# Kernel tuning notes

Hardware: AMD Instinct MI355X
Metric: run time of the kernel (lower is better)

## Reference

```python
import jax, jax.numpy as jnp
import numpy as np

B = 64            # graphs
N0 = 1024         # nodes per graph at level 0
DEG = 16          # avg degree
D = 128
NS = [1024, 820, 656, 525, 420, 336]  # ceil(0.8*n) cascade


def gcn(x, src, dst, valid, W, b, num_nodes):
    # x: [N,D]; src/dst: [E] int; valid: [E] float mask; W: [D,D]; b: [D]
    x = x @ W.T + b
    deg = jax.ops.segment_sum(valid, src, num_segments=num_nodes) + 1.0  # +1 self loop
    dis = jax.lax.rsqrt(deg)
    norm = dis[src] * dis[dst] * valid
    agg = jax.ops.segment_sum(norm[:, None] * x[src], dst, num_segments=num_nodes)
    return agg + (dis * dis)[:, None] * x  # self-loop term


def topk_pool(x, src, dst, valid, w, n, k):
    # PyG TopKPooling: score = tanh((x.w)/||w||); keep top ceil(ratio*n) per graph
    s = jnp.tanh((x @ w) / jnp.linalg.norm(w))
    _, idx = jax.lax.top_k(s.reshape(B, n), k)                    # [B,k] local ids
    perm = (idx + (jnp.arange(B) * n)[:, None]).reshape(-1)       # global ids
    xn = x[perm] * s[perm][:, None]
    new_id = jnp.full((B * n,), -1, jnp.int32).at[perm].set(jnp.arange(B * k, dtype=jnp.int32))
    ns_, nd_ = new_id[src], new_id[dst]
    v = valid * ((ns_ >= 0) & (nd_ >= 0)).astype(jnp.float32)
    return xn, jnp.maximum(ns_, 0), jnp.maximum(nd_, 0), v


def setup_inputs() -> dict:
    key = jax.random.key(0)
    ks = jax.random.split(key, 32)
    x = jax.random.normal(ks[0], (B * N0, D), jnp.float32)
    eg = N0 * DEG  # edges per graph
    local = jax.random.randint(ks[1], (2, B, eg), 0, N0, jnp.int32)
    edge_index = (local + (jnp.arange(B, dtype=jnp.int32) * N0)[None, :, None]).reshape(2, -1)
    batch = jnp.repeat(jnp.arange(B, dtype=jnp.int32), N0)
    sc = 1.0 / np.sqrt(D)
    inp = {"x": x, "edge_index": edge_index, "batch": batch}
    for i in range(1, 6):
        inp[f"c{i}w"] = jax.random.normal(ks[2 * i], (D, D), jnp.float32) * sc
        inp[f"c{i}b"] = jnp.zeros((D,), jnp.float32)
        inp[f"p{i}w"] = jax.random.normal(ks[2 * i + 1], (D,), jnp.float32) * sc
    inp["l1w"] = jax.random.normal(ks[20], (128, 256), jnp.float32) / np.sqrt(256)
    inp["l1b"] = jnp.zeros((128,), jnp.float32)
    inp["l2w"] = jax.random.normal(ks[21], (64, 128), jnp.float32) * sc
    inp["l2b"] = jnp.zeros((64,), jnp.float32)
    inp["l3w"] = jax.random.normal(ks[22], (2, 64), jnp.float32) / np.sqrt(64)
    inp["l3b"] = jnp.zeros((2,), jnp.float32)
    return inp


def reference(x, edge_index, batch,
              c1w, c1b, p1w, c2w, c2b, p2w, c3w, c3b, p3w,
              c4w, c4b, p4w, c5w, c5b, p5w,
              l1w, l1b, l2w, l2b, l3w, l3b):
    src, dst = edge_index[0], edge_index[1]
    valid = jnp.ones(src.shape, jnp.float32)
    layers = [(c1w, c1b, p1w), (c2w, c2b, p2w), (c3w, c3b, p3w),
              (c4w, c4b, p4w), (c5w, c5b, p5w)]
    reads = []
    for i, (cw, cb, pw) in enumerate(layers):
        n, k = NS[i], NS[i + 1]
        x = jax.nn.relu(gcn(x, src, dst, valid, cw, cb, B * n))
        x, src, dst, valid = topk_pool(x, src, dst, valid, pw, n, k)
        xk = x.reshape(B, k, D)
        reads.append(jnp.concatenate([xk.max(axis=1), xk.mean(axis=1)], axis=1))
    h = reads[0] + reads[1] + reads[2] + reads[3] + reads[4]   # [B,256]
    h = jax.nn.relu(h @ l1w.T + l1b)
    # dropout is identity in eval mode
    h = jax.nn.relu(h @ l2w.T + l2b)
    return jax.nn.log_softmax(h @ l3w.T + l3b, axis=-1)       # [B,2]
```

## Files before the change

### kernel.cpp

```cpp
#include <hip/hip_runtime.h>
#include <math.h>

#define NB 64
#define DIM 128
#define ETOT 1048576
#define EPG 16384
#define EPT 16
#define WRS 192
#define XRS 96

static const int NS_H[6] = {1024, 820, 656, 525, 420, 336};

__global__ __launch_bounds__(1024) void init_kernel(const int* __restrict__ ei,
                                  int* __restrict__ src, int* __restrict__ dst,
                                  int2* __restrict__ epack, int* __restrict__ eoff,
                                  int* __restrict__ cnt, float* __restrict__ dinv,
                                  float* __restrict__ invn, const float* __restrict__ pw0,
                                  float* __restrict__ hsum) {
    __shared__ int hs[1024], hc[1024], cur[1024];
    __shared__ float dv[1024];
    __shared__ float shf[128];
    __shared__ int wsum[16];
    int g = blockIdx.x, t = threadIdx.x;
    int lane = t & 63, wv = t >> 6;
    hs[t] = 0; hc[t] = 0;
    if (t < 256) hsum[g * 256 + t] = 0.f;
    __syncthreads();
    int b0 = g * EPG;
    int sr[EPT], dr[EPT];
#pragma unroll
    for (int q = 0; q < EPT; q++) {
        int e = b0 + q * 1024 + t;
        int s = ei[e], d = ei[ETOT + e];
        sr[q] = s; dr[q] = d;
        src[e] = s; dst[e] = d;
        atomicAdd(&hs[s & 1023], 1);
        atomicAdd(&hc[d & 1023], 1);
    }
    __syncthreads();
    int v = hc[t];
    dv[t] = rsqrtf((float)hs[t] + 1.0f);
    int s = v;
#pragma unroll
    for (int off = 1; off < 64; off <<= 1) {
        int u = __shfl_up(s, off, 64);
        if (lane >= off) s += u;
    }
    if (lane == 63) wsum[wv] = s;
    __syncthreads();
    if (wv == 0) {
        int ws = (lane < 16) ? wsum[lane] : 0;
#pragma unroll
        for (int off = 1; off < 16; off <<= 1) {
            int u = __shfl_up(ws, off, 64);
            if (lane >= off) ws += u;
        }
        if (lane < 16) wsum[lane] = ws;
    }
    __syncthreads();
    int excl = b0 + s + ((wv > 0) ? wsum[wv - 1] : 0) - v;
    eoff[g * 1024 + t] = excl;
    cnt[g * 1024 + t] = v;
    dinv[g * 1024 + t] = dv[t];
    cur[t] = excl;
    __syncthreads();
#pragma unroll
    for (int q = 0; q < EPT; q++) {
        int sl = sr[q] & 1023, dl = dr[q] & 1023;
        int pos = atomicAdd(&cur[dl], 1);
        epack[pos] = make_int2(sr[q], __float_as_int(dv[sl] * dv[dl]));
    }
    if (g == 0) {
        if (t < 128) shf[t] = pw0[t] * pw0[t];
        __syncthreads();
        for (int q = 64; q > 0; q >>= 1) {
            if (t < q) shf[t] += shf[t + q];
            __syncthreads();
        }
        if (t == 0) invn[0] = rsqrtf(shf[0]);
    }
}

__global__ __launch_bounds__(256) void linear_kernel(const float* __restrict__ x,
                              const float* __restrict__ W, const float* __restrict__ b,
                              float* __restrict__ y, int N) {
    __shared__ float Wt[32 * WRS];
    __shared__ float xT[32 * XRS];
    int tid = threadIdx.x;
    int base = blockIdx.x * 64;
    int nf = tid & 15;
    int u  = tid >> 4;
    float acc[4][8];
    {
        float bv[8];
#pragma unroll
        for (int f = 0; f < 8; f++) bv[f] = b[u * 8 + f];
#pragma unroll
        for (int i = 0; i < 4; i++)
#pragma unroll
            for (int f = 0; f < 8; f++) acc[i][f] = bv[f];
    }
    for (int kb = 0; kb < 4; kb++) {
        __syncthreads();
#pragma unroll
        for (int q = 0; q < 4; q++) {
            int i = q * 256 + tid;
            int dq = i >> 7;
            int r = i & 127;
            int s = (r >> 3) * 12 + (r & 7);
            float4 wv = *(const float4*)(W + r * 128 + kb * 32 + dq * 4);
            Wt[(dq * 4 + 0) * WRS + s] = wv.x;
            Wt[(dq * 4 + 1) * WRS + s] = wv.y;
            Wt[(dq * 4 + 2) * WRS + s] = wv.z;
            Wt[(dq * 4 + 3) * WRS + s] = wv.w;
        }
#pragma unroll
        for (int q = 0; q < 2; q++) {
            int i = q * 256 + tid;
            int dq = i >> 6;
            int r = i & 63;
            int s = (r >> 3) * 12 + (r & 7);
            float4 xv = *(const float4*)(x + (size_t)(base + r) * DIM + kb * 32 + dq * 4);
            xT[(dq * 4 + 0) * XRS + s] = xv.x;
            xT[(dq * 4 + 1) * XRS + s] = xv.y;
            xT[(dq * 4 + 2) * XRS + s] = xv.z;
            xT[(dq * 4 + 3) * XRS + s] = xv.w;
        }
        __syncthreads();
#pragma unroll 4
        for (int d = 0; d < 32; d++) {
            float4 xv = *(const float4*)&xT[d * XRS + (nf >> 1) * 12 + (nf & 1) * 4];
            float4 wa = *(const float4*)&Wt[d * WRS + u * 12];
            float4 wb = *(const float4*)&Wt[d * WRS + u * 12 + 4];
            float xs[4] = {xv.x, xv.y, xv.z, xv.w};
            float ws[8] = {wa.x, wa.y, wa.z, wa.w, wb.x, wb.y, wb.z, wb.w};
#pragma unroll
            for (int i = 0; i < 4; i++)
#pragma unroll
                for (int f = 0; f < 8; f++)
                    acc[i][f] += xs[i] * ws[f];
        }
    }
#pragma unroll
    for (int i = 0; i < 4; i++) {
        int nd = base + nf * 4 + i;
        float* yp = y + (size_t)nd * DIM + u * 8;
        *(float4*)(yp + 0) = make_float4(acc[i][0], acc[i][1], acc[i][2], acc[i][3]);
        *(float4*)(yp + 4) = make_float4(acc[i][4], acc[i][5], acc[i][6], acc[i][7]);
    }
}

__global__ void fused_agg_kernel(const float* __restrict__ xL, const int2* __restrict__ epack,
                                 const int* __restrict__ eoff, const int* __restrict__ cnt,
                                 const float* __restrict__ dinv,
                                 const float* __restrict__ pw, const float* __restrict__ invn,
                                 float* __restrict__ xA, float* __restrict__ score, int n) {
    int t = threadIdx.x;
    int g = blockIdx.x % NB;
    int chunk = blockIdx.x / NB;
    int ln = chunk * 8 + (t >> 5);
    if (ln >= n) return;
    int node = g * n + ln;
    int lane = t & 31;
    float dsn = dinv[node];
    float4 sv = ((const float4*)(xL + (size_t)node * DIM))[lane];
    float w0 = dsn * dsn;
    float4 a0 = make_float4(sv.x * w0, sv.y * w0, sv.z * w0, sv.w * w0);
    float4 a1 = make_float4(0.f, 0.f, 0.f, 0.f);
    float4 a2 = make_float4(0.f, 0.f, 0.f, 0.f);
    float4 a3 = make_float4(0.f, 0.f, 0.f, 0.f);
    int s0 = eoff[node], s1 = s0 + cnt[node];
    int j = s0;
    int2 e0, e1, e2, e3;
    if (j + 3 < s1) { e0 = epack[j]; e1 = epack[j + 1]; e2 = epack[j + 2]; e3 = epack[j + 3]; }
    for (; j + 7 < s1; j += 4) {
        int2 f0 = epack[j + 4], f1 = epack[j + 5], f2 = epack[j + 6], f3 = epack[j + 7];
        float4 x0 = ((const float4*)(xL + (size_t)e0.x * DIM))[lane];
        float4 x1 = ((const float4*)(xL + (size_t)e1.x * DIM))[lane];
        float4 x2 = ((const float4*)(xL + (size_t)e2.x * DIM))[lane];
        float4 x3 = ((const float4*)(xL + (size_t)e3.x * DIM))[lane];
        float n0 = __int_as_float(e0.y), n1 = __int_as_float(e1.y);
        float n2 = __int_as_float(e2.y), n3 = __int_as_float(e3.y);
        a0.x += n0 * x0.x; a0.y += n0 * x0.y; a0.z += n0 * x0.z; a0.w += n0 * x0.w;
        a1.x += n1 * x1.x; a1.y += n1 * x1.y; a1.z += n1 * x1.z; a1.w += n1 * x1.w;
        a2.x += n2 * x2.x; a2.y += n2 * x2.y; a2.z += n2 * x2.z; a2.w += n2 * x2.w;
        a3.x += n3 * x3.x; a3.y += n3 * x3.y; a3.z += n3 * x3.z; a3.w += n3 * x3.w;
        e0 = f0; e1 = f1; e2 = f2; e3 = f3;
    }
    if (j + 3 < s1) {
        float4 x0 = ((const float4*)(xL + (size_t)e0.x * DIM))[lane];
        float4 x1 = ((const float4*)(xL + (size_t)e1.x * DIM))[lane];
        float4 x2 = ((const float4*)(xL + (size_t)e2.x * DIM))[lane];
        float4 x3 = ((const float4*)(xL + (size_t)e3.x * DIM))[lane];
        float n0 = __int_as_float(e0.y), n1 = __int_as_float(e1.y);
        float n2 = __int_as_float(e2.y), n3 = __int_as_float(e3.y);
        a0.x += n0 * x0.x; a0.y += n0 * x0.y; a0.z += n0 * x0.z; a0.w += n0 * x0.w;
        a1.x += n1 * x1.x; a1.y += n1 * x1.y; a1.z += n1 * x1.z; a1.w += n1 * x1.w;
        a2.x += n2 * x2.x; a2.y += n2 * x2.y; a2.z += n2 * x2.z; a2.w += n2 * x2.w;
        a3.x += n3 * x3.x; a3.y += n3 * x3.y; a3.z += n3 * x3.z; a3.w += n3 * x3.w;
        j += 4;
    }
    for (; j < s1; j++) {
        int2 eq = epack[j];
        float nq = __int_as_float(eq.y);
        float4 xq = ((const float4*)(xL + (size_t)eq.x * DIM))[lane];
        a0.x += nq * xq.x; a0.y += nq * xq.y; a0.z += nq * xq.z; a0.w += nq * xq.w;
    }
    float4 acc = make_float4(fmaxf(a0.x + a1.x + a2.x + a3.x, 0.f),
                             fmaxf(a0.y + a1.y + a2.y + a3.y, 0.f),
                             fmaxf(a0.z + a1.z + a2.z + a3.z, 0.f),
                             fmaxf(a0.w + a1.w + a2.w + a3.w, 0.f));
    ((float4*)(xA + (size_t)node * DIM))[lane] = acc;
    float4 pv = ((const float4*)pw)[lane];
    float dot = acc.x * pv.x + acc.y * pv.y + acc.z * pv.z + acc.w * pv.w;
    for (int off = 16; off >= 1; off >>= 1) dot += __shfl_xor(dot, off, 32);
    if (lane == 0) score[node] = tanhf(dot * invn[0]);
}

__global__ __launch_bounds__(1024) void pool_kernel(const float* __restrict__ score,
                              const float* __restrict__ xA, float* __restrict__ xn,
                              float* __restrict__ h, int* __restrict__ src,
                              int* __restrict__ dst, int2* __restrict__ epack,
                              int* __restrict__ eoff, int* __restrict__ cnt,
                              float* __restrict__ dinv, const float* __restrict__ pwN,
                              float* __restrict__ invn, int n, int k, int last,
                              const float* __restrict__ l1w, const float* __restrict__ l1b,
                              const float* __restrict__ l2w, const float* __restrict__ l2b,
                              const float* __restrict__ l3w, const float* __restrict__ l3b,
                              float* __restrict__ out) {
    __shared__ float keyS[2][1024];
    __shared__ int idxS[2][1024];
    __shared__ int nid[1024];
    __shared__ float4 smax[32][33];
    __shared__ float4 ssum[32][33];
    __shared__ int hs[1024], hc[1024], cur[1024];
    __shared__ float dv[1024];
    __shared__ float shf[128];
    __shared__ int wsum[16];
    __shared__ float hr[256], h1[128], h2[64], lz[2];
    int g = blockIdx.x, t = threadIdx.x;
    int lane = t & 63, wv = t >> 6;
    int b0 = g * EPG, gn = g * n, gk = g * k;
    float k_r = (t < n) ? score[g * n + t] : -2.0f;
    int i_r = t;
    hs[t] = 0; hc[t] = 0;
    int se[EPT], de[EPT];
    if (!last) {
#pragma unroll
        for (int q = 0; q < EPT; q++) {
            int e = b0 + q * 1024 + t;
            se[q] = src[e];
            de[q] = dst[e];
        }
    }
    int par = 0;
    for (unsigned ksz = 2; ksz <= 1024; ksz <<= 1) {
        for (unsigned jj = ksz >> 1; jj > 0; jj >>= 1) {
            float kq; int iq;
            if (jj >= 64) {
                keyS[par][t] = k_r; idxS[par][t] = i_r;
                __syncthreads();
                kq = keyS[par][t ^ jj]; iq = idxS[par][t ^ jj];
                par ^= 1;
            } else {
                kq = __shfl_xor(k_r, (int)jj, 64);
                iq = __shfl_xor(i_r, (int)jj, 64);
            }
            bool mineFirst = (k_r > kq) || (k_r == kq && i_r < iq);
            bool up = ((t & ksz) == 0);
            bool iAmLower = ((t & jj) == 0);
            bool keepMine = (iAmLower == up) ? mineFirst : !mineFirst;
            if (!keepMine) { k_r = kq; i_r = iq; }
        }
    }
    keyS[0][t] = k_r; idxS[0][t] = i_r;
    nid[i_r] = (t < (unsigned)k) ? t : -1;
    __syncthreads();
    int lane4 = t & 31;
    int ch = t >> 5;
    float4 mx = make_float4(-INFINITY, -INFINITY, -INFINITY, -INFINITY);
    float4 sm = make_float4(0.f, 0.f, 0.f, 0.f);
    for (int j = ch; j < k; j += 32) {
        int row = idxS[0][j];
        float sval = keyS[0][j];
        float4 vv = ((const float4*)(xA + ((size_t)g * n + row) * DIM))[lane4];
        vv.x *= sval; vv.y *= sval; vv.z *= sval; vv.w *= sval;
        if (!last) ((float4*)(xn + ((size_t)g * k + j) * DIM))[lane4] = vv;
        mx.x = fmaxf(mx.x, vv.x); mx.y = fmaxf(mx.y, vv.y);
        mx.z = fmaxf(mx.z, vv.z); mx.w = fmaxf(mx.w, vv.w);
        sm.x += vv.x; sm.y += vv.y; sm.z += vv.z; sm.w += vv.w;
    }
    smax[ch][lane4] = mx;
    ssum[ch][lane4] = sm;
    __syncthreads();
    for (int s = 16; s >= 1; s >>= 1) {
        if (ch < s) {
            float4 a = smax[ch][lane4], bb = smax[ch + s][lane4];
            a.x = fmaxf(a.x, bb.x); a.y = fmaxf(a.y, bb.y);
            a.z = fmaxf(a.z, bb.z); a.w = fmaxf(a.w, bb.w);
            smax[ch][lane4] = a;
            float4 c = ssum[ch][lane4], d = ssum[ch + s][lane4];
            c.x += d.x; c.y += d.y; c.z += d.z; c.w += d.w;
            ssum[ch][lane4] = c;
        }
        __syncthreads();
    }
    if (ch == 0) {
        float4 m = smax[0][lane4];
        float4 s4 = ssum[0][lane4];
        float invk = 1.0f / (float)k;
        int f0 = lane4 * 4;
        if (!last) {
            float* hp = h + g * 256;
            hp[f0 + 0] += m.x; hp[f0 + 1] += m.y; hp[f0 + 2] += m.z; hp[f0 + 3] += m.w;
            hp[128 + f0 + 0] += s4.x * invk; hp[128 + f0 + 1] += s4.y * invk;
            hp[128 + f0 + 2] += s4.z * invk; hp[128 + f0 + 3] += s4.w * invk;
        } else {
            const float* hp = h + g * 256;
            hr[f0 + 0] = hp[f0 + 0] + m.x; hr[f0 + 1] = hp[f0 + 1] + m.y;
            hr[f0 + 2] = hp[f0 + 2] + m.z; hr[f0 + 3] = hp[f0 + 3] + m.w;
            hr[128 + f0 + 0] = hp[128 + f0 + 0] + s4.x * invk;
            hr[128 + f0 + 1] = hp[128 + f0 + 1] + s4.y * invk;
            hr[128 + f0 + 2] = hp[128 + f0 + 2] + s4.z * invk;
            hr[128 + f0 + 3] = hp[128 + f0 + 3] + s4.w * invk;
        }
    }
    if (last) {
        __syncthreads();
        if (t < 128) {
            float a1 = l1b[t];
            for (int d = 0; d < 256; d++) a1 += hr[d] * l1w[t * 256 + d];
            h1[t] = fmaxf(a1, 0.f);
        }
        __syncthreads();
        if (t < 64) {
            float a2 = l2b[t];
            for (int d = 0; d < 128; d++) a2 += h1[d] * l2w[t * 128 + d];
            h2[t] = fmaxf(a2, 0.f);
        }
        __syncthreads();
        if (t < 2) {
            float a3 = l3b[t];
            for (int d = 0; d < 64; d++) a3 += h2[d] * l3w[t * 64 + d];
            lz[t] = a3;
        }
        __syncthreads();
        if (t < 2) {
            float z0 = lz[0], z1 = lz[1];
            float m = fmaxf(z0, z1);
            float lse = m + logf(expf(z0 - m) + expf(z1 - m));
            out[g * 2 + t] = lz[t] - lse;
        }
        return;
    }
    int sr[EPT], dr[EPT];
#pragma unroll
    for (int q = 0; q < EPT; q++) {
        int e = b0 + q * 1024 + t;
        int s = se[q];
        int s2 = -1, d2 = -1;
        if (s >= 0) {
            s2 = nid[s - gn];
            d2 = nid[de[q] - gn];
            if (s2 >= 0 && d2 >= 0) {
                src[e] = gk + s2;
                dst[e] = gk + d2;
                atomicAdd(&hs[s2], 1);
                atomicAdd(&hc[d2], 1);
            } else {
                src[e] = -1;
                dst[e] = -1;
                s2 = -1;
            }
        }
        sr[q] = s2; dr[q] = d2;
    }
    __syncthreads();
    int v = (t < k) ? hc[t] : 0;
    if (t < k) dv[t] = rsqrtf((float)hs[t] + 1.0f);
    int s = v;
#pragma unroll
    for (int off = 1; off < 64; off <<= 1) {
        int u = __shfl_up(s, off, 64);
        if (lane >= off) s += u;
    }
    if (lane == 63) wsum[wv] = s;
    __syncthreads();
    if (wv == 0) {
        int ws = (lane < 16) ? wsum[lane] : 0;
#pragma unroll
        for (int off = 1; off < 16; off <<= 1) {
            int u = __shfl_up(ws, off, 64);
            if (lane >= off) ws += u;
        }
        if (lane < 16) wsum[lane] = ws;
    }
    __syncthreads();
    if (t < k) {
        int excl = b0 + s + ((wv > 0) ? wsum[wv - 1] : 0) - v;
        eoff[gk + t] = excl;
        cnt[gk + t] = v;
        dinv[gk + t] = dv[t];
        cur[t] = excl;
    }
    __syncthreads();
#pragma unroll
    for (int q = 0; q < EPT; q++) {
        if (sr[q] >= 0) {
            int pos = atomicAdd(&cur[dr[q]], 1);
            epack[pos] = make_int2(gk + sr[q], __float_as_int(dv[sr[q]] * dv[dr[q]]));
        }
    }
    if (g == 0) {
        if (t < 128) shf[t] = pwN[t] * pwN[t];
        __syncthreads();
        for (int q = 64; q > 0; q >>= 1) {
            if (t < q) shf[t] += shf[t + q];
            __syncthreads();
        }
        if (t == 0) invn[0] = rsqrtf(shf[0]);
    }
}

extern "C" void kernel_launch(void* const* d_in, const int* in_sizes, int n_in,
                              void* d_out, int out_size, void* d_ws, size_t ws_size,
                              hipStream_t stream) {
    const float* x_in = (const float*)d_in[0];
    const int* edge_index = (const int*)d_in[1];
    const float *cw[5], *cb[5], *pw[5];
    for (int i = 0; i < 5; i++) {
        cw[i] = (const float*)d_in[3 + 3 * i];
        cb[i] = (const float*)d_in[4 + 3 * i];
        pw[i] = (const float*)d_in[5 + 3 * i];
    }
    const float* l1w = (const float*)d_in[18];
    const float* l1b = (const float*)d_in[19];
    const float* l2w = (const float*)d_in[20];
    const float* l2b = (const float*)d_in[21];
    const float* l3w = (const float*)d_in[22];
    const float* l3b = (const float*)d_in[23];
    float* out = (float*)d_out;

    char* w = (char*)d_ws;
    float* xA    = (float*)w; w += (size_t)65536 * DIM * 4;
    float* xB    = (float*)w; w += (size_t)65536 * DIM * 4;
    float* xL    = (float*)w; w += (size_t)65536 * DIM * 4;
    int*   src   = (int*)w;   w += (size_t)ETOT * 4;
    int*   dst   = (int*)w;   w += (size_t)ETOT * 4;
    int2*  epack = (int2*)w;  w += (size_t)ETOT * 8;
    int*   cnt   = (int*)w;   w += (size_t)65536 * 4;
    int*   eoff  = (int*)w;   w += (size_t)65536 * 4;
    float* dinv  = (float*)w; w += (size_t)65536 * 4;
    float* score = (float*)w; w += (size_t)65536 * 4;
    float* hsum  = (float*)w; w += (size_t)NB * 256 * 4;
    float* invn  = (float*)w; w += 4;

    init_kernel<<<NB, 1024, 0, stream>>>(edge_index, src, dst, epack, eoff, cnt, dinv,
                                         invn, pw[0], hsum);

    const float* xin = x_in;
    for (int i = 0; i < 5; i++) {
        int n = NS_H[i], k = NS_H[i + 1];
        int N = NB * n;

        linear_kernel<<<N / 64, 256, 0, stream>>>(xin, cw[i], cb[i], xL, N);
        int gpb = (n + 7) / 8;
        fused_agg_kernel<<<NB * gpb, 256, 0, stream>>>(xL, epack, eoff, cnt, dinv, pw[i],
                                                       invn, xA, score, n);
        pool_kernel<<<NB, 1024, 0, stream>>>(score, xA, xB, hsum, src, dst, epack, eoff,
                                             cnt, dinv, (i < 4) ? pw[i + 1] : pw[i], invn,
                                             n, k, (i == 4) ? 1 : 0,
                                             l1w, l1b, l2w, l2b, l3w, l3b, out);

        xin = xB;
    }
}
```

Before: 530.0 us.

## Store linear output in fp16 to halve neighbor gather traffic

The linear kernel now writes its transformed features as half precision, and the aggregation kernel gathers neighbor rows as 8-byte half4 loads and converts them to float before accumulating. This halves the bytes moved by the irregular per-edge gathers, which dominate the aggregation cost. The aggregated output is also written with a nontemporal store. In exchange, intermediate features are rounded to fp16, which may affect accuracy and the top-k ordering.

```diff
diff --git a/kernel.cpp b/kernel.cpp
--- a/kernel.cpp
+++ b/kernel.cpp
@@ -1,4 +1,5 @@
 #include <hip/hip_runtime.h>
+#include <hip/hip_fp16.h>
 #include <math.h>
 
 #define NB 64
@@ -10,6 +11,8 @@
 #define XRS 96
 
 static const int NS_H[6] = {1024, 820, 656, 525, 420, 336};
+
+typedef float f4v __attribute__((ext_vector_type(4)));
 
 __global__ __launch_bounds__(1024) void init_kernel(const int* __restrict__ ei,
                                   int* __restrict__ src, int* __restrict__ dst,
@@ -83,7 +86,7 @@
 
 __global__ __launch_bounds__(256) void linear_kernel(const float* __restrict__ x,
                               const float* __restrict__ W, const float* __restrict__ b,
-                              float* __restrict__ y, int N) {
+                              __half* __restrict__ xH, int N) {
     __shared__ float Wt[32 * WRS];
     __shared__ float xT[32 * XRS];
     int tid = threadIdx.x;
@@ -144,13 +147,16 @@
 #pragma unroll
     for (int i = 0; i < 4; i++) {
         int nd = base + nf * 4 + i;
-        float* yp = y + (size_t)nd * DIM + u * 8;
-        *(float4*)(yp + 0) = make_float4(acc[i][0], acc[i][1], acc[i][2], acc[i][3]);
-        *(float4*)(yp + 4) = make_float4(acc[i][4], acc[i][5], acc[i][6], acc[i][7]);
+        alignas(16) __half2 hb[4];
+        hb[0] = __floats2half2_rn(acc[i][0], acc[i][1]);
+        hb[1] = __floats2half2_rn(acc[i][2], acc[i][3]);
+        hb[2] = __floats2half2_rn(acc[i][4], acc[i][5]);
+        hb[3] = __floats2half2_rn(acc[i][6], acc[i][7]);
+        *(float4*)(xH + (size_t)nd * DIM + u * 8) = *(const float4*)hb;
     }
 }
 
-__global__ void fused_agg_kernel(const float* __restrict__ xL, const int2* __restrict__ epack,
+__global__ void fused_agg_kernel(const __half* __restrict__ xH, const int2* __restrict__ epack,
                                  const int* __restrict__ eoff, const int* __restrict__ cnt,
                                  const float* __restrict__ dinv,
                                  const float* __restrict__ pw, const float* __restrict__ invn,
@@ -163,9 +169,11 @@
     int node = g * n + ln;
     int lane = t & 31;
     float dsn = dinv[node];
-    float4 sv = ((const float4*)(xL + (size_t)node * DIM))[lane];
+    uint2 qs = ((const uint2*)(xH + (size_t)node * DIM))[lane];
+    float2 sl = __half22float2(*(const __half2*)&qs.x);
+    float2 sh = __half22float2(*(const __half2*)&qs.y);
     float w0 = dsn * dsn;
-    float4 a0 = make_float4(sv.x * w0, sv.y * w0, sv.z * w0, sv.w * w0);
+    float4 a0 = make_float4(sl.x * w0, sl.y * w0, sh.x * w0, sh.y * w0);
     float4 a1 = make_float4(0.f, 0.f, 0.f, 0.f);
     float4 a2 = make_float4(0.f, 0.f, 0.f, 0.f);
     float4 a3 = make_float4(0.f, 0.f, 0.f, 0.f);
@@ -175,42 +183,52 @@
     if (j + 3 < s1) { e0 = epack[j]; e1 = epack[j + 1]; e2 = epack[j + 2]; e3 = epack[j + 3]; }
     for (; j + 7 < s1; j += 4) {
         int2 f0 = epack[j + 4], f1 = epack[j + 5], f2 = epack[j + 6], f3 = epack[j + 7];
-        float4 x0 = ((const float4*)(xL + (size_t)e0.x * DIM))[lane];
-        float4 x1 = ((const float4*)(xL + (size_t)e1.x * DIM))[lane];
-        float4 x2 = ((const float4*)(xL + (size_t)e2.x * DIM))[lane];
-        float4 x3 = ((const float4*)(xL + (size_t)e3.x * DIM))[lane];
+        uint2 x0 = ((const uint2*)(xH + (size_t)e0.x * DIM))[lane];
+        uint2 x1 = ((const uint2*)(xH + (size_t)e1.x * DIM))[lane];
+        uint2 x2 = ((const uint2*)(xH + (size_t)e2.x * DIM))[lane];
+        uint2 x3 = ((const uint2*)(xH + (size_t)e3.x * DIM))[lane];
         float n0 = __int_as_float(e0.y), n1 = __int_as_float(e1.y);
         float n2 = __int_as_float(e2.y), n3 = __int_as_float(e3.y);
-        a0.x += n0 * x0.x; a0.y += n0 * x0.y; a0.z += n0 * x0.z; a0.w += n0 * x0.w;
-        a1.x += n1 * x1.x; a1.y += n1 * x1.y; a1.z += n1 * x1.z; a1.w += n1 * x1.w;
-        a2.x += n2 * x2.x; a2.y += n2 * x2.y; a2.z += n2 * x2.z; a2.w += n2 * x2.w;
-        a3.x += n3 * x3.x; a3.y += n3 * x3.y; a3.z += n3 * x3.z; a3.w += n3 * x3.w;
+        float2 l0 = __half22float2(*(const __half2*)&x0.x), h0 = __half22float2(*(const __half2*)&x0.y);
+        float2 l1 = __half22float2(*(const __half2*)&x1.x), h1 = __half22float2(*(const __half2*)&x1.y);
+        float2 l2 = __half22float2(*(const __half2*)&x2.x), h2 = __half22float2(*(const __half2*)&x2.y);
+        float2 l3 = __half22float2(*(const __half2*)&x3.x), h3 = __half22float2(*(const __half2*)&x3.y);
+        a0.x += n0 * l0.x; a0.y += n0 * l0.y; a0.z += n0 * h0.x; a0.w += n0 * h0.y;
+        a1.x += n1 * l1.x; a1.y += n1 * l1.y; a1.z += n1 * h1.x; a1.w += n1 * h1.y;
+        a2.x += n2 * l2.x; a2.y += n2 * l2.y; a2.z += n2 * h2.x; a2.w += n2 * h2.y;
+        a3.x += n3 * l3.x; a3.y += n3 * l3.y; a3.z += n3 * h3.x; a3.w += n3 * h3.y;
         e0 = f0; e1 = f1; e2 = f2; e3 = f3;
     }
     if (j + 3 < s1) {
-        float4 x0 = ((const float4*)(xL + (size_t)e0.x * DIM))[lane];
-        float4 x1 = ((const float4*)(xL + (size_t)e1.x * DIM))[lane];
-        float4 x2 = ((const float4*)(xL + (size_t)e2.x * DIM))[lane];
-        float4 x3 = ((const float4*)(xL + (size_t)e3.x * DIM))[lane];
+        uint2 x0 = ((const uint2*)(xH + (size_t)e0.x * DIM))[lane];
+        uint2 x1 = ((const uint2*)(xH + (size_t)e1.x * DIM))[lane];
+        uint2 x2 = ((const uint2*)(xH + (size_t)e2.x * DIM))[lane];
+        uint2 x3 = ((const uint2*)(xH + (size_t)e3.x * DIM))[lane];
         float n0 = __int_as_float(e0.y), n1 = __int_as_float(e1.y);
         float n2 = __int_as_float(e2.y), n3 = __int_as_float(e3.y);
-        a0.x += n0 * x0.x; a0.y += n0 * x0.y; a0.z += n0 * x0.z; a0.w += n0 * x0.w;
-        a1.x += n1 * x1.x; a1.y += n1 * x1.y; a1.z += n1 * x1.z; a1.w += n1 * x1.w;
-        a2.x += n2 * x2.x; a2.y += n2 * x2.y; a2.z += n2 * x2.z; a2.w += n2 * x2.w;
-        a3.x += n3 * x3.x; a3.y += n3 * x3.y; a3.z += n3 * x3.z; a3.w += n3 * x3.w;
+        float2 l0 = __half22float2(*(const __half2*)&x0.x), h0 = __half22float2(*(const __half2*)&x0.y);
+        float2 l1 = __half22float2(*(const __half2*)&x1.x), h1 = __half22float2(*(const __half2*)&x1.y);
+        float2 l2 = __half22float2(*(const __half2*)&x2.x), h2 = __half22float2(*(const __half2*)&x2.y);
+        float2 l3 = __half22float2(*(const __half2*)&x3.x), h3 = __half22float2(*(const __half2*)&x3.y);
+        a0.x += n0 * l0.x; a0.y += n0 * l0.y; a0.z += n0 * h0.x; a0.w += n0 * h0.y;
+        a1.x += n1 * l1.x; a1.y += n1 * l1.y; a1.z += n1 * h1.x; a1.w += n1 * h1.y;
+        a2.x += n2 * l2.x; a2.y += n2 * l2.y; a2.z += n2 * h2.x; a2.w += n2 * h2.y;
+        a3.x += n3 * l3.x; a3.y += n3 * l3.y; a3.z += n3 * h3.x; a3.w += n3 * h3.y;
         j += 4;
     }
     for (; j < s1; j++) {
         int2 eq = epack[j];
         float nq = __int_as_float(eq.y);
-        float4 xq = ((const float4*)(xL + (size_t)eq.x * DIM))[lane];
-        a0.x += nq * xq.x; a0.y += nq * xq.y; a0.z += nq * xq.z; a0.w += nq * xq.w;
+        uint2 xq = ((const uint2*)(xH + (size_t)eq.x * DIM))[lane];
+        float2 lq = __half22float2(*(const __half2*)&xq.x), hq = __half22float2(*(const __half2*)&xq.y);
+        a0.x += nq * lq.x; a0.y += nq * lq.y; a0.z += nq * hq.x; a0.w += nq * hq.y;
     }
     float4 acc = make_float4(fmaxf(a0.x + a1.x + a2.x + a3.x, 0.f),
                              fmaxf(a0.y + a1.y + a2.y + a3.y, 0.f),
                              fmaxf(a0.z + a1.z + a2.z + a3.z, 0.f),
                              fmaxf(a0.w + a1.w + a2.w + a3.w, 0.f));
-    ((float4*)(xA + (size_t)node * DIM))[lane] = acc;
+    f4v av; av[0] = acc.x; av[1] = acc.y; av[2] = acc.z; av[3] = acc.w;
+    __builtin_nontemporal_store(av, (f4v*)(xA + (size_t)node * DIM + lane * 4));
     float4 pv = ((const float4*)pw)[lane];
     float dot = acc.x * pv.x + acc.y * pv.y + acc.z * pv.z + acc.w * pv.w;
     for (int off = 16; off >= 1; off >>= 1) dot += __shfl_xor(dot, off, 32);
@@ -444,7 +462,7 @@
     char* w = (char*)d_ws;
     float* xA    = (float*)w; w += (size_t)65536 * DIM * 4;
     float* xB    = (float*)w; w += (size_t)65536 * DIM * 4;
-    float* xL    = (float*)w; w += (size_t)65536 * DIM * 4;
+    __half* xH   = (__half*)w; w += (size_t)65536 * DIM * 4;
     int*   src   = (int*)w;   w += (size_t)ETOT * 4;
     int*   dst   = (int*)w;   w += (size_t)ETOT * 4;
     int2*  epack = (int2*)w;  w += (size_t)ETOT * 8;
@@ -463,9 +481,9 @@
         int n = NS_H[i], k = NS_H[i + 1];
         int N = NB * n;
 
-        linear_kernel<<<N / 64, 256, 0, stream>>>(xin, cw[i], cb[i], xL, N);
+        linear_kernel<<<N / 64, 256, 0, stream>>>(xin, cw[i], cb[i], xH, N);
         int gpb = (n + 7) / 8;
-        fused_agg_kernel<<<NB * gpb, 256, 0, stream>>>(xL, epack, eoff, cnt, dinv, pw[i],
+        fused_agg_kernel<<<NB * gpb, 256, 0, stream>>>(xH, epack, eoff, cnt, dinv, pw[i],
                                                        invn, xA, score, n);
         pool_kernel<<<NB, 1024, 0, stream>>>(score, xA, xB, hsum, src, dst, epack, eoff,
                                              cnt, dinv, (i < 4) ? pw[i + 1] : pw[i], invn,
```

After: 542.0 us. 2.3% more time.
